# Performance work log

Measured on AMD Instinct MI355X. Metric: run time of the kernel, lower is better.

## Reference

```python
import jax, jax.numpy as jnp
import numpy as np

R = 128            # dense leaf-grid resolution (stand-in for N^3 octree leaves)
N_STEPS = 192      # fixed marching budget (replaces data-dependent while loop)
STEP_SIZE = 0.001
BACKGROUND = 1.0
DELTA_SCALE = 1.0  # 1/invradius with tree radius 1


def setup_inputs() -> dict:
    key = jax.random.key(0)
    k1, k2, k3, k4 = jax.random.split(key, 4)
    B = 65536
    grid = jax.random.normal(k1, (R, R, R, 4), dtype=jnp.float32)
    origins = jax.random.uniform(k2, (B, 3), dtype=jnp.float32)          # inside unit cube
    dirs = jax.random.normal(k3, (B, 3), dtype=jnp.float32)
    viewdirs = jax.random.normal(k4, (B, 3), dtype=jnp.float32)
    return {"grid": grid, "origins": origins, "dirs": dirs, "viewdirs": viewdirs}


def _dda_unit(cen, invdir):
    # entry/exit of ray cen + t*dir vs the unit cube [0,1]^3
    t1 = -cen * invdir            # [B,3]
    t2 = t1 + invdir
    lo = jnp.minimum(t1, t2)
    hi = jnp.maximum(t1, t2)
    tmin = jnp.maximum(jnp.max(lo, axis=-1), 0.0)   # [B]
    tmax = jnp.minimum(jnp.min(hi, axis=-1), 1e9)   # [B]
    return tmin, tmax


def _render(grid, origins, dirs, viewdirs):
    del viewdirs  # RGBA data_format: no SH basis evaluation
    dirs = dirs / jnp.linalg.norm(dirs, axis=-1, keepdims=True)
    invdirs = 1.0 / (dirs + 1e-9)
    t, tmax = _dda_unit(origins, invdirs)
    B = origins.shape[0]
    light = jnp.ones((B,), dtype=origins.dtype)
    out_rgb = jnp.zeros((B, 3), dtype=origins.dtype)
    cube_sz = 1.0 / R

    def step(carry, _):
        t, light, out_rgb = carry
        active = t < tmax
        pos = origins + t[:, None] * dirs                      # [B,3]
        idxf = jnp.floor(pos * R)
        idx = jnp.clip(idxf.astype(jnp.int32), 0, R - 1)       # voxel index
        rgba = grid[idx[:, 0], idx[:, 1], idx[:, 2]]           # [B,4] gather
        pos_t = pos * R - idx.astype(pos.dtype)                # local coords in voxel
        smin, smax = _dda_unit(pos_t, invdirs)
        delta_t = (smax - smin) * cube_sz + STEP_SIZE          # [B]
        sigma = jax.nn.relu(rgba[:, 3])
        att = jnp.exp(-delta_t * sigma * DELTA_SCALE)
        weight = light * (1.0 - att)
        rgb = jax.nn.sigmoid(rgba[:, :3])
        out_rgb = out_rgb + jnp.where(active[:, None], weight[:, None] * rgb, 0.0)
        light = jnp.where(active, light * att, light)
        t = jnp.where(active, t + delta_t, t)
        return (t, light, out_rgb), None

    (t, light, out_rgb), _ = jax.lax.scan(step, (t, light, out_rgb), None, length=N_STEPS)
    return out_rgb + BACKGROUND * light[:, None]


def reference(grid, origins, dirs, viewdirs):
    return _render(grid, origins, dirs, viewdirs)
```

## Files before the change

kernel.cpp:

```cpp
#include <hip/hip_runtime.h>


constexpr int   R_DIM    = 128;
constexpr int   N_VOX    = R_DIM * R_DIM * R_DIM;
constexpr int   N_STEPS  = 192;
constexpr int   PASSES   = N_STEPS / 64;
constexpr float STEP_SZ  = 0.001f;
constexpr float CUBE_SZ  = 1.0f / 128.0f;
constexpr float SIG_MAX  = 5.5f;
constexpr int   PIPE     = 8;
constexpr int   CVT_BLOCKS = (N_VOX / 4 + 255) / 256;

__device__ __forceinline__ float sigmoid_fast(float x) {
    return __builtin_amdgcn_rcpf(1.0f + __expf(-x));
}

__device__ __forceinline__ void geom_step(
    float tl, float tmax,
    float oxR, float oyR, float ozR, float dxR, float dyR, float dzR,
    float ix, float iy, float iz, float ipx, float ipy, float ipz,
    int& i0, int& i1, int& i2, float& d)
{
    float px = __fadd_rn(oxR, __fmul_rn(tl, dxR));
    float py = __fadd_rn(oyR, __fmul_rn(tl, dyR));
    float pz = __fadd_rn(ozR, __fmul_rn(tl, dzR));

    float c0 = fminf(fmaxf(floorf(px), 0.0f), 127.0f);
    float c1 = fminf(fmaxf(floorf(py), 0.0f), 127.0f);
    float c2 = fminf(fmaxf(floorf(pz), 0.0f), 127.0f);
    i0 = (int)c0;
    i1 = (int)c1;
    i2 = (int)c2;

    float t1x = __fmul_rn(__fsub_rn(c0, px), ix);
    float t1y = __fmul_rn(__fsub_rn(c1, py), iy);
    float t1z = __fmul_rn(__fsub_rn(c2, pz), iz);
    float hix = __fadd_rn(t1x, ipx);
    float hiy = __fadd_rn(t1y, ipy);
    float hiz = __fadd_rn(t1z, ipz);
    float smax = fminf(fminf(fminf(hix, hiy), hiz), 1e9f);

    d = __fadd_rn(__fmul_rn(smax, CUBE_SZ), STEP_SZ);
    d = (tl < tmax) ? d : 0.0f;
}

__device__ __forceinline__ void ray_setup(
    const float* __restrict__ origins, const float* __restrict__ dirs, int i,
    float& oxR, float& oyR, float& ozR, float& dxR, float& dyR, float& dzR,
    float& ix, float& iy, float& iz,
    float& ipx, float& ipy, float& ipz,
    float& tmin, float& tmax)
{
    float ox = origins[3 * i + 0];
    float oy = origins[3 * i + 1];
    float oz = origins[3 * i + 2];
    float dx = dirs[3 * i + 0];
    float dy = dirs[3 * i + 1];
    float dz = dirs[3 * i + 2];

    float n2 = __fadd_rn(__fadd_rn(__fmul_rn(dx, dx), __fmul_rn(dy, dy)),
                         __fmul_rn(dz, dz));
    float nrm = sqrtf(n2);
    dx = dx / nrm;
    dy = dy / nrm;
    dz = dz / nrm;

    ix = 1.0f / __fadd_rn(dx, 1e-9f);
    iy = 1.0f / __fadd_rn(dy, 1e-9f);
    iz = 1.0f / __fadd_rn(dz, 1e-9f);

    ipx = fmaxf(ix, 0.0f);
    ipy = fmaxf(iy, 0.0f);
    ipz = fmaxf(iz, 0.0f);

    float t1x = __fmul_rn(-ox, ix), t2x = __fadd_rn(t1x, ix);
    float t1y = __fmul_rn(-oy, iy), t2y = __fadd_rn(t1y, iy);
    float t1z = __fmul_rn(-oz, iz), t2z = __fadd_rn(t1z, iz);
    float lox = fminf(t1x, t2x), hix = fmaxf(t1x, t2x);
    float loy = fminf(t1y, t2y), hiy = fmaxf(t1y, t2y);
    float loz = fminf(t1z, t2z), hiz = fmaxf(t1z, t2z);
    tmin = fmaxf(fmaxf(fmaxf(lox, loy), loz), 0.0f);
    tmax = fminf(fminf(fminf(hix, hiy), hiz), 1e9f);

    oxR = __fmul_rn(ox, 128.0f);
    oyR = __fmul_rn(oy, 128.0f);
    ozR = __fmul_rn(oz, 128.0f);
    dxR = __fmul_rn(dx, 128.0f);
    dyR = __fmul_rn(dy, 128.0f);
    dzR = __fmul_rn(dz, 128.0f);
}

__device__ __forceinline__ unsigned pack_voxel(float4 v) {
    unsigned ur = (unsigned)__float2int_rn(sigmoid_fast(v.x) * 255.0f);
    unsigned ug = (unsigned)__float2int_rn(sigmoid_fast(v.y) * 255.0f);
    unsigned ub = (unsigned)__float2int_rn(sigmoid_fast(v.z) * 255.0f);
    unsigned us = (unsigned)__float2int_rn(
        fminf(fmaxf(v.w, 0.0f), SIG_MAX) * (255.0f / SIG_MAX));
    return ur | (ug << 8) | (ub << 16) | (us << 24);
}

__global__ __launch_bounds__(256) void prep(
    const float4* __restrict__ g, uint4* __restrict__ gq4,
    const float* __restrict__ origins, const float* __restrict__ dirs,
    float* __restrict__ tarr, int B, int walk_blocks)
{
    if ((int)blockIdx.x < walk_blocks) {
        int r = blockIdx.x * 256 + threadIdx.x;
        if (r >= B) return;

        float oxR, oyR, ozR, dxR, dyR, dzR, ix, iy, iz, ipx, ipy, ipz;
        float tmin, tmax;
        ray_setup(origins, dirs, r, oxR, oyR, ozR, dxR, dyR, dzR,
                  ix, iy, iz, ipx, ipy, ipz, tmin, tmax);

        float t = tmin;
        float4* dst = (float4*)&tarr[(size_t)r * N_STEPS];
        for (int c = 0; c < N_STEPS / PIPE; ++c) {
            float buf[PIPE];
            #pragma unroll
            for (int p = 0; p < PIPE; ++p) {
                buf[p] = t;
                int i0, i1, i2; float d;
                geom_step(t, tmax, oxR, oyR, ozR, dxR, dyR, dzR,
                          ix, iy, iz, ipx, ipy, ipz, i0, i1, i2, d);
                t = __fadd_rn(t, d);
            }
            dst[2 * c + 0] = make_float4(buf[0], buf[1], buf[2], buf[3]);
            dst[2 * c + 1] = make_float4(buf[4], buf[5], buf[6], buf[7]);
        }
        return;
    }

    int tid = (blockIdx.x - walk_blocks) * 256 + threadIdx.x;
    if (tid >= N_VOX / 4) return;
    int zq = tid & 31;
    int y  = (tid >> 5) & 127;
    int x  = tid >> 12;

    int src = (x * R_DIM + y) * R_DIM + 4 * zq;
    float4 v0 = g[src + 0];
    float4 v1 = g[src + 1];
    float4 v2 = g[src + 2];
    float4 v3 = g[src + 3];

    uint4 o;
    o.x = pack_voxel(v0);
    o.y = pack_voxel(v1);
    o.z = pack_voxel(v2);
    o.w = pack_voxel(v3);

    int bid = ((x >> 2) << 10) | ((y >> 2) << 5) | zq;
    int dst = bid * 16 + (x & 3) * 4 + (y & 3);
    gq4[dst] = o;
}

__global__ __launch_bounds__(256, 8) void volrend_scan(
    const unsigned int* __restrict__ gq,
    const float* __restrict__ tarr,
    const float* __restrict__ origins,
    const float* __restrict__ dirs,
    float* __restrict__ out,
    int B)
{
    int lane = threadIdx.x & 63;
    int wid  = threadIdx.x >> 6;
    int r = blockIdx.x * 4 + wid;
    if (r >= B) return;

    float oxR, oyR, ozR, dxR, dyR, dzR, ix, iy, iz, ipx, ipy, ipz, tmin, tmax;
    ray_setup(origins, dirs, r, oxR, oyR, ozR, dxR, dyR, dzR,
              ix, iy, iz, ipx, ipy, ipz, tmin, tmax);
    (void)tmin;

    float tv[PASSES], del[PASSES];
    unsigned val[PASSES];
    #pragma unroll
    for (int p = 0; p < PASSES; ++p)
        tv[p] = tarr[(size_t)r * N_STEPS + p * 64 + lane];
    #pragma unroll
    for (int p = 0; p < PASSES; ++p) {
        int i0, i1, i2; float d;
        geom_step(tv[p], tmax, oxR, oyR, ozR, dxR, dyR, dzR,
                  ix, iy, iz, ipx, ipy, ipz, i0, i1, i2, d);
        unsigned bid = ((unsigned)(i0 >> 2) << 10) |
                       ((unsigned)(i1 >> 2) << 5) |
                       (unsigned)(i2 >> 2);
        unsigned loc = ((unsigned)(i0 & 3) << 4) |
                       ((unsigned)(i1 & 3) << 2) |
                       (unsigned)(i2 & 3);
        val[p] = gq[(bid << 6) | loc];
        del[p] = d;
    }

    float light = 1.0f;
    float ar = 0.0f, ag = 0.0f, ab = 0.0f;

    #pragma unroll
    for (int p = 0; p < PASSES; ++p) {
        unsigned v = val[p];
        float sg  = (float)(v >> 24);
        float a   = __expf(del[p] * (-SIG_MAX / 255.0f) * sg);
        float P = a;
        #pragma unroll
        for (int s = 1; s < 64; s <<= 1) {
            float q = __shfl_up(P, s, 64);
            P *= (lane >= s) ? q : 1.0f;
        }
        float E = __shfl_up(P, 1, 64);
        E = (lane == 0) ? 1.0f : E;
        float w = light * E * (1.0f - a) * (1.0f / 255.0f);
        ar = fmaf(w, (float)(v & 255u),         ar);
        ag = fmaf(w, (float)((v >> 8) & 255u),  ag);
        ab = fmaf(w, (float)((v >> 16) & 255u), ab);
        light *= __shfl(P, 63, 64);
    }

    #pragma unroll
    for (int m = 32; m >= 1; m >>= 1) {
        ar += __shfl_xor(ar, m, 64);
        ag += __shfl_xor(ag, m, 64);
        ab += __shfl_xor(ab, m, 64);
    }
    if (lane == 0) {
        out[3 * r + 0] = ar + light;
        out[3 * r + 1] = ag + light;
        out[3 * r + 2] = ab + light;
    }
}

__global__ __launch_bounds__(256) void volrend_f32(
    const float* __restrict__ grid,
    const float* __restrict__ origins,
    const float* __restrict__ dirs,
    float* __restrict__ out,
    int B)
{
    int i = blockIdx.x * blockDim.x + threadIdx.x;
    if (i >= B) return;

    float oxR, oyR, ozR, dxR, dyR, dzR, ix, iy, iz, ipx, ipy, ipz, tmin, tmax;
    ray_setup(origins, dirs, i, oxR, oyR, ozR, dxR, dyR, dzR,
              ix, iy, iz, ipx, ipy, ipz, tmin, tmax);

    const float4* __restrict__ g4 = (const float4*)grid;

    float t = tmin;
    float light = 1.0f;
    float ar = 0.0f, ag = 0.0f, ab = 0.0f;

    for (int chunk = 0; chunk < N_STEPS / PIPE; ++chunk) {
        if (t >= tmax) break;

        float4 val[PIPE];
        float del[PIPE];
        float tl = t;

        #pragma unroll
        for (int p = 0; p < PIPE; ++p) {
            int i0, i1, i2; float d;
            geom_step(tl, tmax, oxR, oyR, ozR, dxR, dyR, dzR,
                      ix, iy, iz, ipx, ipy, ipz, i0, i1, i2, d);
            val[p] = g4[(i0 * R_DIM + i1) * R_DIM + i2];
            del[p] = d;
            tl = __fadd_rn(tl, d);
        }

        #pragma unroll
        for (int p = 0; p < PIPE; ++p) {
            float sigma = fmaxf(val[p].w, 0.0f);
            float att = __expf(-del[p] * sigma);
            float w = light * (1.0f - att);
            ar = fmaf(w, sigmoid_fast(val[p].x), ar);
            ag = fmaf(w, sigmoid_fast(val[p].y), ag);
            ab = fmaf(w, sigmoid_fast(val[p].z), ab);
            light *= att;
        }

        t = tl;
    }

    out[3 * i + 0] = ar + light;
    out[3 * i + 1] = ag + light;
    out[3 * i + 2] = ab + light;
}

extern "C" void kernel_launch(void* const* d_in, const int* in_sizes, int n_in,
                              void* d_out, int out_size, void* d_ws, size_t ws_size,
                              hipStream_t stream) {
    const float* grid    = (const float*)d_in[0];
    const float* origins = (const float*)d_in[1];
    const float* dirs    = (const float*)d_in[2];
    float* out = (float*)d_out;

    int B = in_sizes[1] / 3;

    size_t need = (size_t)N_VOX * 4 + (size_t)B * N_STEPS * 4;
    if (ws_size >= need && (B % 64) == 0) {
        uint4* gq4  = (uint4*)d_ws;
        float* tarr = (float*)((char*)d_ws + (size_t)N_VOX * 4);
        int walk_blocks = (B + 255) / 256;
        prep<<<walk_blocks + CVT_BLOCKS, 256, 0, stream>>>(
            (const float4*)grid, gq4, origins, dirs, tarr, B, walk_blocks);
        volrend_scan<<<B / 4, 256, 0, stream>>>(
            (const unsigned int*)gq4, tarr, origins, dirs, out, B);
    } else {
        volrend_f32<<<(B + 255) / 256, 256, 0, stream>>>(grid, origins, dirs,
                                                         out, B);
    }
}
```

Measured before the change: 133.4 us.

## Store t checkpoints every 3 steps and composite with segment-wise scan

The prep pass now stores only every third t value in a coalesced [checkpoint][ray] layout and stops early once every ray in the wave has exited. The render kernel has each of the 64 lanes recompute three consecutive steps from its checkpoint and composite them locally. Lane segments are then combined with a single associative (color, transmittance) scan, replacing the per-pass prefix-product scans and the final reductions. This cuts workspace traffic and shuffle work, at the cost of recomputing geometry in the render kernel and a serial 3-step dependency per lane.

```diff
diff --git a/kernel.cpp b/kernel.cpp
--- a/kernel.cpp
+++ b/kernel.cpp
@@ -4,7 +4,8 @@
 constexpr int   R_DIM    = 128;
 constexpr int   N_VOX    = R_DIM * R_DIM * R_DIM;
 constexpr int   N_STEPS  = 192;
-constexpr int   PASSES   = N_STEPS / 64;
+constexpr int   CP_LEN   = 3;
+constexpr int   N_CP     = N_STEPS / CP_LEN;
 constexpr float STEP_SZ  = 0.001f;
 constexpr float CUBE_SZ  = 1.0f / 128.0f;
 constexpr float SIG_MAX  = 5.5f;
@@ -102,7 +103,7 @@
 __global__ __launch_bounds__(256) void prep(
     const float4* __restrict__ g, uint4* __restrict__ gq4,
     const float* __restrict__ origins, const float* __restrict__ dirs,
-    float* __restrict__ tarr, int B, int walk_blocks)
+    float* __restrict__ cp, int B, int walk_blocks)
 {
     if ((int)blockIdx.x < walk_blocks) {
         int r = blockIdx.x * 256 + threadIdx.x;
@@ -114,19 +115,20 @@
                   ix, iy, iz, ipx, ipy, ipz, tmin, tmax);
 
         float t = tmin;
-        float4* dst = (float4*)&tarr[(size_t)r * N_STEPS];
-        for (int c = 0; c < N_STEPS / PIPE; ++c) {
-            float buf[PIPE];
+        for (int c = 0; c < N_CP; ++c) {
+            cp[(size_t)c * B + r] = t;
             #pragma unroll
-            for (int p = 0; p < PIPE; ++p) {
-                buf[p] = t;
+            for (int p = 0; p < CP_LEN; ++p) {
                 int i0, i1, i2; float d;
                 geom_step(t, tmax, oxR, oyR, ozR, dxR, dyR, dzR,
                           ix, iy, iz, ipx, ipy, ipz, i0, i1, i2, d);
                 t = __fadd_rn(t, d);
             }
-            dst[2 * c + 0] = make_float4(buf[0], buf[1], buf[2], buf[3]);
-            dst[2 * c + 1] = make_float4(buf[4], buf[5], buf[6], buf[7]);
+            if (__all(t >= tmax)) {
+                for (int cc = c + 1; cc < N_CP; ++cc)
+                    cp[(size_t)cc * B + r] = t;
+                break;
+            }
         }
         return;
     }
@@ -154,9 +156,9 @@
     gq4[dst] = o;
 }
 
-__global__ __launch_bounds__(256, 8) void volrend_scan(
+__global__ __launch_bounds__(256, 8) void volrend_lane3(
     const unsigned int* __restrict__ gq,
-    const float* __restrict__ tarr,
+    const float* __restrict__ cp,
     const float* __restrict__ origins,
     const float* __restrict__ dirs,
     float* __restrict__ out,
@@ -172,15 +174,14 @@
               ix, iy, iz, ipx, ipy, ipz, tmin, tmax);
     (void)tmin;
 
-    float tv[PASSES], del[PASSES];
-    unsigned val[PASSES];
+    float t = cp[(size_t)lane * B + r];
+
+    float light = 1.0f;
+    float ar = 0.0f, ag = 0.0f, ab = 0.0f;
     #pragma unroll
-    for (int p = 0; p < PASSES; ++p)
-        tv[p] = tarr[(size_t)r * N_STEPS + p * 64 + lane];
-    #pragma unroll
-    for (int p = 0; p < PASSES; ++p) {
+    for (int p = 0; p < CP_LEN; ++p) {
         int i0, i1, i2; float d;
-        geom_step(tv[p], tmax, oxR, oyR, ozR, dxR, dyR, dzR,
+        geom_step(t, tmax, oxR, oyR, ozR, dxR, dyR, dzR,
                   ix, iy, iz, ipx, ipy, ipz, i0, i1, i2, d);
         unsigned bid = ((unsigned)(i0 >> 2) << 10) |
                        ((unsigned)(i1 >> 2) << 5) |
@@ -188,39 +189,34 @@
         unsigned loc = ((unsigned)(i0 & 3) << 4) |
                        ((unsigned)(i1 & 3) << 2) |
                        (unsigned)(i2 & 3);
-        val[p] = gq[(bid << 6) | loc];
-        del[p] = d;
-    }
-
-    float light = 1.0f;
-    float ar = 0.0f, ag = 0.0f, ab = 0.0f;
-
-    #pragma unroll
-    for (int p = 0; p < PASSES; ++p) {
-        unsigned v = val[p];
-        float sg  = (float)(v >> 24);
-        float a   = __expf(del[p] * (-SIG_MAX / 255.0f) * sg);
-        float P = a;
-        #pragma unroll
-        for (int s = 1; s < 64; s <<= 1) {
-            float q = __shfl_up(P, s, 64);
-            P *= (lane >= s) ? q : 1.0f;
-        }
-        float E = __shfl_up(P, 1, 64);
-        E = (lane == 0) ? 1.0f : E;
-        float w = light * E * (1.0f - a) * (1.0f / 255.0f);
+        unsigned v = gq[(bid << 6) | loc];
+        float sg = (float)(v >> 24);
+        float a  = __expf(d * (-SIG_MAX / 255.0f) * sg);
+        float w  = light * (1.0f - a) * (1.0f / 255.0f);
         ar = fmaf(w, (float)(v & 255u),         ar);
         ag = fmaf(w, (float)((v >> 8) & 255u),  ag);
         ab = fmaf(w, (float)((v >> 16) & 255u), ab);
-        light *= __shfl(P, 63, 64);
+        light *= a;
+        t = __fadd_rn(t, d);
     }
 
     #pragma unroll
-    for (int m = 32; m >= 1; m >>= 1) {
-        ar += __shfl_xor(ar, m, 64);
-        ag += __shfl_xor(ag, m, 64);
-        ab += __shfl_xor(ab, m, 64);
-    }
+    for (int s = 1; s < 64; s <<= 1) {
+        float arn = __shfl_down(ar,    s, 64);
+        float agn = __shfl_down(ag,    s, 64);
+        float abn = __shfl_down(ab,    s, 64);
+        float ltn = __shfl_down(light, s, 64);
+        bool ok = (lane + s) < 64;
+        arn = ok ? arn : 0.0f;
+        agn = ok ? agn : 0.0f;
+        abn = ok ? abn : 0.0f;
+        ltn = ok ? ltn : 1.0f;
+        ar = fmaf(light, arn, ar);
+        ag = fmaf(light, agn, ag);
+        ab = fmaf(light, abn, ab);
+        light *= ltn;
+    }
+
     if (lane == 0) {
         out[3 * r + 0] = ar + light;
         out[3 * r + 1] = ag + light;
@@ -294,15 +290,15 @@
 
     int B = in_sizes[1] / 3;
 
-    size_t need = (size_t)N_VOX * 4 + (size_t)B * N_STEPS * 4;
+    size_t need = (size_t)N_VOX * 4 + (size_t)N_CP * B * 4;
     if (ws_size >= need && (B % 64) == 0) {
-        uint4* gq4  = (uint4*)d_ws;
-        float* tarr = (float*)((char*)d_ws + (size_t)N_VOX * 4);
+        uint4* gq4 = (uint4*)d_ws;
+        float* cp  = (float*)((char*)d_ws + (size_t)N_VOX * 4);
         int walk_blocks = (B + 255) / 256;
         prep<<<walk_blocks + CVT_BLOCKS, 256, 0, stream>>>(
-            (const float4*)grid, gq4, origins, dirs, tarr, B, walk_blocks);
-        volrend_scan<<<B / 4, 256, 0, stream>>>(
-            (const unsigned int*)gq4, tarr, origins, dirs, out, B);
+            (const float4*)grid, gq4, origins, dirs, cp, B, walk_blocks);
+        volrend_lane3<<<B / 4, 256, 0, stream>>>(
+            (const unsigned int*)gq4, cp, origins, dirs, out, B);
     } else {
         volrend_f32<<<(B + 255) / 256, 256, 0, stream>>>(grid, origins, dirs,
                                                          out, B);
```

New measurement: 136.4 us. 2.2% more time.
